# Kernel tuning notes

Hardware: AMD Instinct MI355X
Metric: run time of the kernel (lower is better)

The kernel has to match this reference:

```python
import jax, jax.numpy as jnp
import numpy as np

BLANK = 0  # blank_id from init_kwargs


def _rnnt_prefix(logp, tgt, tl):
    """RNN-T prefix-search DP (verbose variant, B==1).
    logp: [T, U, D] log-softmaxed logits; tgt: [U] int; tl: scalar int (target length).
    Returns per-frame (log_alpha_t [T], start_t [T], total_t [T]) as float32.
    Recurrence: alpha[t,0]=0 (new start at frame t);
      alpha[0,u] = alpha[0,u-1] + logp[0,u-1,tgt[u-1]];
      alpha[t,u] = max(alpha[t-1,u] + logp[t-1,u,blank],  # stay (blank)
                       alpha[t,u-1] + logp[t,u-1,tgt[u-1]])  # emit label
    with >= tie-break preferring the blank (left) path, tracking start frame
    and total path length alongside.
    """
    T, U, D = logp.shape
    dt = logp.dtype
    # emit[t,u] = logp[t,u,tgt[u]]  (used as the u-1 term)
    emit = jnp.take_along_axis(logp, tgt[None, :, None].astype(jnp.int32), axis=2)[..., 0]  # [T,U]
    blk = logp[:, :, BLANK]            # [T,U]
    blk_tl = blk[:, tl]                # [T], blank prob at column target_len

    # ----- t == 0 row -----
    alpha0 = jnp.concatenate([jnp.zeros((1,), dt), jnp.cumsum(emit[0, :U - 1])])
    start0 = jnp.zeros((U,), dt)
    total0 = jnp.arange(1, U + 1, dtype=dt)

    def row_step(carry, x):
        a_d, s_d, t_d = carry          # alpha/start/total at (t, u-1)
        fla, fls, fltot, e = x         # from-left candidates + emit[t, u-1]
        fd = a_d + e                   # from-down score
        left = fla >= fd               # tie-break prefers left (blank) path
        a = jnp.where(left, fla, fd)
        s = jnp.where(left, fls, s_d)
        tt = jnp.where(left, fltot, t_d) + 1.0
        return (a, s, tt), (a, s, tt)

    def t_step(carry, x):
        pa, ps, pt = carry             # previous row (t-1): alpha/start/total [U]
        blk_prev, emit_row, btl, tval = x
        a0 = jnp.zeros((), dt)         # alpha[t,0] = 0: fresh start at frame t
        s0 = tval
        tot0 = jnp.ones((), dt)
        xs = (pa[1:] + blk_prev[1:], ps[1:], pt[1:], emit_row[:U - 1])
        _, (ar, sr, tr) = jax.lax.scan(row_step, (a0, s0, tot0), xs)
        alpha = jnp.concatenate([a0[None], ar])
        start = jnp.concatenate([s0[None], sr])
        total = jnp.concatenate([tot0[None], tr])
        out = (alpha[tl] + btl, start[tl], total[tl] + 1.0)
        return (alpha, start, total), out

    ts = jnp.arange(1, T, dtype=dt)
    xs = (blk[:T - 1], emit[1:], blk_tl[1:], ts)
    _, (la_r, st_r, to_r) = jax.lax.scan(t_step, (alpha0, start0, total0), xs)

    la = jnp.concatenate([(alpha0[tl] + blk_tl[0])[None], la_r])
    st = jnp.concatenate([start0[tl][None], st_r])
    to = jnp.concatenate([(total0[tl] + 1.0)[None], to_r])
    return la, st, to


def setup_inputs() -> dict:
    T, U, D = 2000, 32, 4096
    key = jax.random.key(0)
    k1, k2 = jax.random.split(key)
    logits = jax.random.normal(k1, (1, T, U, D), dtype=jnp.float32)
    targets = jax.random.randint(k2, (1, U), 1, D)  # labels in [1, D), avoid blank=0
    logit_lens = jnp.full((1,), T, dtype=jnp.int32)   # accepted but unused by the math
    target_lens = jnp.full((1,), U - 1, dtype=jnp.int32)
    return {"logits": logits, "targets": targets,
            "logit_lens": logit_lens, "target_lens": target_lens}


def reference(logits, targets, logit_lens, target_lens):
    logp = jax.nn.log_softmax(logits, axis=-1)
    la, st, to = _rnnt_prefix(logp[0], targets[0], target_lens[0])
    # (forward_logprob at last frame, log_alpha per t, start per t, total per t)
    return (la[-1], la, st.astype(jnp.int32), to.astype(jnp.int32))
```

## Files before the change

kernel.cpp:

```cpp
#include <hip/hip_runtime.h>
#include <math.h>

#define TDIM 2000
#define UDIM 32
#define DDIM 4096
#define NROWS (TDIM * UDIM)
#define NSTEP 2032
#define NPAD  2080

__device__ __forceinline__ int dpp_up1_i(int x) {
    return __builtin_amdgcn_update_dpp(x, x, 0x138, 0xf, 0xf, false);
}
__device__ __forceinline__ float dpp_up1_f(float x) {
    return __int_as_float(dpp_up1_i(__float_as_int(x)));
}

__device__ __forceinline__ void st_agent(float* p, float v) {
    __hip_atomic_store(p, v, __ATOMIC_RELAXED, __HIP_MEMORY_SCOPE_AGENT);
}

__global__ __launch_bounds__(256) void k_fused(
    const float* __restrict__ logits, const int* __restrict__ tgt,
    float* __restrict__ dD, unsigned* __restrict__ cnt,
    const int* __restrict__ tlenp, float* __restrict__ out)
{
    __shared__ float2 lds_out[NSTEP + 64];
    __shared__ float redm[4];
    __shared__ float reds[4];

    if (blockIdx.x != 0) {
        const int r = (int)blockIdx.x - 1;
        const int t = r >> 5;
        const int u = r & (UDIM - 1);
        const float* row = logits + (size_t)r * DDIM;
        const float4* row4 = reinterpret_cast<const float4*>(row);
        const int tid = threadIdx.x;

        float4 x0 = row4[tid];
        float4 x1 = row4[tid + 256];
        float4 x2 = row4[tid + 512];
        float4 x3 = row4[tid + 768];

        float m = fmaxf(fmaxf(fmaxf(x0.x, x0.y), fmaxf(x0.z, x0.w)),
                   fmaxf(fmaxf(fmaxf(x1.x, x1.y), fmaxf(x1.z, x1.w)),
                    fmaxf(fmaxf(fmaxf(x2.x, x2.y), fmaxf(x2.z, x2.w)),
                          fmaxf(fmaxf(x3.x, x3.y), fmaxf(x3.z, x3.w)))));
        #pragma unroll
        for (int off = 32; off > 0; off >>= 1)
            m = fmaxf(m, __shfl_xor(m, off));

        const int wid = tid >> 6, lane = tid & 63;
        if (lane == 0) redm[wid] = m;
        __syncthreads();
        m = fmaxf(fmaxf(redm[0], redm[1]), fmaxf(redm[2], redm[3]));

        float s = 0.f;
        s += expf(x0.x - m) + expf(x0.y - m) + expf(x0.z - m) + expf(x0.w - m);
        s += expf(x1.x - m) + expf(x1.y - m) + expf(x1.z - m) + expf(x1.w - m);
        s += expf(x2.x - m) + expf(x2.y - m) + expf(x2.z - m) + expf(x2.w - m);
        s += expf(x3.x - m) + expf(x3.y - m) + expf(x3.z - m) + expf(x3.w - m);
        #pragma unroll
        for (int off = 32; off > 0; off >>= 1)
            s += __shfl_xor(s, off);
        if (lane == 0) reds[wid] = s;
        __syncthreads();

        if (tid == 0) {
            float tot = (reds[0] + reds[1]) + (reds[2] + reds[3]);
            float l = logf(tot);
            float b = (x0.x - m) - l;
            float e = (row[tgt[u]] - m) - l;
            const int n = t + u + 1;
            st_agent(&dD[(n * UDIM + u) * 2], b);
            if (u < UDIM - 1)
                st_agent(&dD[(n * UDIM + u + 1) * 2 + 1], e);
            asm volatile("s_waitcnt vmcnt(0)" ::: "memory");
            __hip_atomic_fetch_add(&cnt[n], 1u, __ATOMIC_RELAXED,
                                   __HIP_MEMORY_SCOPE_AGENT);
        }
        return;
    }

    const int u = (int)threadIdx.x;

    if (u < 64) {
        const int tl = tlenp[0];
        const bool is_tl = (u == tl);
        const int trash = NSTEP + u;
        const float2* dj = (const float2*)dD;

        {
            int n_ = u & 31;
            int hi_ = min(31, n_ - 1);
            int lo_ = max(0, n_ - 2000);
            unsigned exp_ = (unsigned)max(0, hi_ - lo_ + 1);
            if (exp_) {
                while (__hip_atomic_load(&cnt[n_], __ATOMIC_RELAXED,
                                         __HIP_MEMORY_SCOPE_AGENT) < exp_) {}
            }
            asm volatile("" ::: "memory");
        }

        float a = 0.f;
        int   p = 1;

        float2 q0,q1,q2,q3,q4,q5,q6,q7,q8,q9,q10,q11,q12,q13,q14,q15,
               q16,q17,q18,q19,q20,q21,q22,q23,q24,q25,q26,q27,q28,q29,q30,q31;
        q0  = dj[ 0*UDIM+u]; q1  = dj[ 1*UDIM+u];
        q2  = dj[ 2*UDIM+u]; q3  = dj[ 3*UDIM+u];
        q4  = dj[ 4*UDIM+u]; q5  = dj[ 5*UDIM+u];
        q6  = dj[ 6*UDIM+u]; q7  = dj[ 7*UDIM+u];
        q8  = dj[ 8*UDIM+u]; q9  = dj[ 9*UDIM+u];
        q10 = dj[10*UDIM+u]; q11 = dj[11*UDIM+u];
        q12 = dj[12*UDIM+u]; q13 = dj[13*UDIM+u];
        q14 = dj[14*UDIM+u]; q15 = dj[15*UDIM+u];
        q16 = dj[16*UDIM+u]; q17 = dj[17*UDIM+u];
        q18 = dj[18*UDIM+u]; q19 = dj[19*UDIM+u];
        q20 = dj[20*UDIM+u]; q21 = dj[21*UDIM+u];
        q22 = dj[22*UDIM+u]; q23 = dj[23*UDIM+u];
        q24 = dj[24*UDIM+u]; q25 = dj[25*UDIM+u];
        q26 = dj[26*UDIM+u]; q27 = dj[27*UDIM+u];
        q28 = dj[28*UDIM+u]; q29 = dj[29*UDIM+u];
        q30 = dj[30*UDIM+u]; q31 = dj[31*UDIM+u];
        const float2* pref = dj + 32 * UDIM + u;
        int n0 = 0;

#define POLLF do {                                                    \
        int pn_ = n0 + 32 + (u & 15);                                 \
        int hi_ = min(31, pn_ - 1);                                   \
        int lo_ = max(0, pn_ - 2000);                                 \
        unsigned exp_ = (unsigned)max(0, hi_ - lo_ + 1);              \
        if (exp_) {                                                   \
            while (__hip_atomic_load(&cnt[pn_], __ATOMIC_RELAXED,     \
                                     __HIP_MEMORY_SCOPE_AGENT) < exp_) {} \
        }                                                             \
        asm volatile("" ::: "memory");                                \
    } while (0)

#define STEP(J, G, CUR, NXT) do {                                      \
        const int n_ = n0 + (J);                                       \
        const int t_ = n_ - u;                                         \
        float aL_ = dpp_up1_f(a);                                      \
        int   pL_ = dpp_up1_i(p);                                      \
        float fla_ = a + CUR.x;                                        \
        if (G) fla_ = (t_ >= 1) ? fla_ : -INFINITY;                    \
        float fd_ = aL_ + CUR.y;                                       \
        float bt_ = NXT.x;                                             \
        CUR = pref[(J) * UDIM];        \
        bool  left_ = (fla_ >= fd_);            \
        float na_ = left_ ? fla_ : fd_;                                \
        int   np_ = (left_ ? p : pL_) + 1;                             \
        if (u == 0) { na_ = 0.f; np_ = (n_ << 12) + 1; }               \
        a = na_; p = np_;                                              \
        int slot_ = (is_tl && (unsigned)t_ < (unsigned)TDIM) ? t_      \
                                                             : trash;  \
        lds_out[slot_] = make_float2(a + bt_, __int_as_float(p));      \
    } while (0)

#define BLOCK_A(G) do {                                                \
        STEP(0,G,q0,q1);   STEP(1,G,q1,q2);   STEP(2,G,q2,q3);         \
        STEP(3,G,q3,q4);   STEP(4,G,q4,q5);   STEP(5,G,q5,q6);         \
        STEP(6,G,q6,q7);   STEP(7,G,q7,q8);   STEP(8,G,q8,q9);         \
        STEP(9,G,q9,q10);  STEP(10,G,q10,q11);STEP(11,G,q11,q12);      \
        STEP(12,G,q12,q13);STEP(13,G,q13,q14);STEP(14,G,q14,q15);      \
        STEP(15,G,q15,q16);                                            \
        pref += 16 * UDIM; n0 += 16;                                   \
    } while (0)

#define BLOCK_B(G) do {                                                \
        STEP(0,G,q16,q17); STEP(1,G,q17,q18); STEP(2,G,q18,q19);       \
        STEP(3,G,q19,q20); STEP(4,G,q20,q21); STEP(5,G,q21,q22);       \
        STEP(6,G,q22,q23); STEP(7,G,q23,q24); STEP(8,G,q24,q25);       \
        STEP(9,G,q25,q26); STEP(10,G,q26,q27);STEP(11,G,q27,q28);      \
        STEP(12,G,q28,q29);STEP(13,G,q29,q30);STEP(14,G,q30,q31);      \
        STEP(15,G,q31,q0);                                             \
        pref += 16 * UDIM; n0 += 16;                                   \
    } while (0)

        for (int it = 0; it < 2; ++it) {
            POLLF; BLOCK_A(1);
            POLLF; BLOCK_B(1);
        }
        for (int it = 0; it < 61; ++it) {
            POLLF; BLOCK_A(0);
            POLLF; BLOCK_B(0);
        }
        POLLF; BLOCK_A(0);

#undef STEP
#undef BLOCK_A
#undef BLOCK_B
#undef POLLF
    }

    __syncthreads();
    for (int t = (int)threadIdx.x; t < TDIM; t += 256) {
        float2 v = lds_out[t];
        int pp = __float_as_int(v.y);
        out[1 + t]            = v.x;
        out[1 + TDIM + t]     = (float)(pp >> 12);
        out[1 + 2 * TDIM + t] = (float)((pp & 4095) + 1);
        if (t == TDIM - 1) out[0] = v.x;
    }
}

extern "C" void kernel_launch(void* const* d_in, const int* in_sizes, int n_in,
                              void* d_out, int out_size, void* d_ws, size_t ws_size,
                              hipStream_t stream)
{
    const float* logits      = (const float*)d_in[0];
    const int*   targets     = (const int*)d_in[1];
    const int*   target_lens = (const int*)d_in[3];
    float* out = (float*)d_out;

    float*    dD  = (float*)d_ws;
    unsigned* cnt = (unsigned*)((char*)d_ws + (size_t)NPAD * UDIM * sizeof(float2));

    hipMemsetAsync(cnt, 0, 2048 * sizeof(unsigned), stream);
    k_fused<<<NROWS + 1, 256, 0, stream>>>(logits, targets, dD, cnt,
                                           target_lens, out);
}
```

Before: 217.8 us.

## Offload global counter polling to a helper wave signaling via LDS flags

A second wavefront in block 0 now polls the global arrival counters for each 16-diagonal batch and publishes readiness through workgroup-scope LDS flags. The DP wavefront only spins on cheap LDS flags instead of issuing agent-scope global atomic loads on its critical path. The aim is to take global-memory poll latency off the serial recurrence. The catch is an extra wave competing for issue slots, plus reliance on the LDS acquire/release ordering to make the global data written by other blocks visible.

Measured after the change: 205.1 us, median of 2. 1.06x faster.

```diff
diff --git a/kernel.cpp b/kernel.cpp
--- a/kernel.cpp
+++ b/kernel.cpp
@@ -7,6 +7,7 @@
 #define NROWS (TDIM * UDIM)
 #define NSTEP 2032
 #define NPAD  2080
+#define NBATCH 129
 
 __device__ __forceinline__ int dpp_up1_i(int x) {
     return __builtin_amdgcn_update_dpp(x, x, 0x138, 0xf, 0xf, false);
@@ -27,6 +28,7 @@
     __shared__ float2 lds_out[NSTEP + 64];
     __shared__ float redm[4];
     __shared__ float reds[4];
+    __shared__ int flags[NBATCH];
 
     if (blockIdx.x != 0) {
         const int r = (int)blockIdx.x - 1;
@@ -81,31 +83,46 @@
         return;
     }
 
-    const int u = (int)threadIdx.x;
-
-    if (u < 64) {
+    const int tid  = (int)threadIdx.x;
+    const int u    = tid & 63;
+    const int wave = tid >> 6;
+
+    if (tid < NBATCH) flags[tid] = 0;
+    __syncthreads();
+
+    if (wave == 1) {
+        for (int w = 0; w < NBATCH; ++w) {
+            int pn_ = w * 16 + (u & 15);
+            int hi_ = min(31, pn_ - 1);
+            int lo_ = max(0, pn_ - 2000);
+            unsigned exp_ = (unsigned)max(0, hi_ - lo_ + 1);
+            if (exp_) {
+                while (__hip_atomic_load(&cnt[pn_], __ATOMIC_RELAXED,
+                                         __HIP_MEMORY_SCOPE_AGENT) < exp_) {}
+            }
+            if (u == 0)
+                __hip_atomic_store(&flags[w], 1, __ATOMIC_RELEASE,
+                                   __HIP_MEMORY_SCOPE_WORKGROUP);
+        }
+    } else if (wave == 0) {
         const int tl = tlenp[0];
         const bool is_tl = (u == tl);
         const int trash = NSTEP + u;
         const float2* dj = (const float2*)dD;
 
-        {
-            int n_ = u & 31;
-            int hi_ = min(31, n_ - 1);
-            int lo_ = max(0, n_ - 2000);
-            unsigned exp_ = (unsigned)max(0, hi_ - lo_ + 1);
-            if (exp_) {
-                while (__hip_atomic_load(&cnt[n_], __ATOMIC_RELAXED,
-                                         __HIP_MEMORY_SCOPE_AGENT) < exp_) {}
-            }
-            asm volatile("" ::: "memory");
-        }
+#define WAITW(W) do {                                                  \
+        while (__hip_atomic_load(&flags[(W)], __ATOMIC_ACQUIRE,        \
+                   __HIP_MEMORY_SCOPE_WORKGROUP) == 0) {}              \
+        asm volatile("" ::: "memory");                                 \
+    } while (0)
 
         float a = 0.f;
         int   p = 1;
 
         float2 q0,q1,q2,q3,q4,q5,q6,q7,q8,q9,q10,q11,q12,q13,q14,q15,
                q16,q17,q18,q19,q20,q21,q22,q23,q24,q25,q26,q27,q28,q29,q30,q31;
+
+        WAITW(0); WAITW(1);
         q0  = dj[ 0*UDIM+u]; q1  = dj[ 1*UDIM+u];
         q2  = dj[ 2*UDIM+u]; q3  = dj[ 3*UDIM+u];
         q4  = dj[ 4*UDIM+u]; q5  = dj[ 5*UDIM+u];
@@ -125,18 +142,6 @@
         const float2* pref = dj + 32 * UDIM + u;
         int n0 = 0;
 
-#define POLLF do {                                                    \
-        int pn_ = n0 + 32 + (u & 15);                                 \
-        int hi_ = min(31, pn_ - 1);                                   \
-        int lo_ = max(0, pn_ - 2000);                                 \
-        unsigned exp_ = (unsigned)max(0, hi_ - lo_ + 1);              \
-        if (exp_) {                                                   \
-            while (__hip_atomic_load(&cnt[pn_], __ATOMIC_RELAXED,     \
-                                     __HIP_MEMORY_SCOPE_AGENT) < exp_) {} \
-        }                                                             \
-        asm volatile("" ::: "memory");                                \
-    } while (0)
-
 #define STEP(J, G, CUR, NXT) do {                                      \
         const int n_ = n0 + (J);                                       \
         const int t_ = n_ - u;                                         \
@@ -178,23 +183,23 @@
     } while (0)
 
         for (int it = 0; it < 2; ++it) {
-            POLLF; BLOCK_A(1);
-            POLLF; BLOCK_B(1);
+            WAITW((n0 >> 4) + 2); BLOCK_A(1);
+            WAITW((n0 >> 4) + 2); BLOCK_B(1);
         }
         for (int it = 0; it < 61; ++it) {
-            POLLF; BLOCK_A(0);
-            POLLF; BLOCK_B(0);
-        }
-        POLLF; BLOCK_A(0);
+            WAITW((n0 >> 4) + 2); BLOCK_A(0);
+            WAITW((n0 >> 4) + 2); BLOCK_B(0);
+        }
+        WAITW((n0 >> 4) + 2); BLOCK_A(0);
 
 #undef STEP
 #undef BLOCK_A
 #undef BLOCK_B
-#undef POLLF
+#undef WAITW
     }
 
     __syncthreads();
-    for (int t = (int)threadIdx.x; t < TDIM; t += 256) {
+    for (int t = tid; t < TDIM; t += 256) {
         float2 v = lds_out[t];
         int pp = __float_as_int(v.y);
         out[1 + t]            = v.x;
```
